# Kernel tuning notes

Measured on AMD Instinct MI355X. Metric: run time of the kernel, lower is better.

## Reference

```python
import jax, jax.numpy as jnp
import numpy as np

N = 50000      # number of genes
E = 1_600_000  # number of GRP edges
F = 256        # feature dim


def setup_inputs() -> dict:
    key = jax.random.key(0)
    k1, k2, k3 = jax.random.split(key, 3)
    indices = jax.random.randint(k1, (2, E), 0, N, dtype=jnp.int64 if jax.config.jax_enable_x64 else jnp.int32)
    values = jax.random.normal(k2, (E,), dtype=jnp.float32)
    mat_2 = jax.random.normal(k3, (N, F), dtype=jnp.float32)
    return {"indices": indices, "values": values, "n": N, "mat_2": mat_2}


def reference(indices, values, n, mat_2):
    # Sparse COO [n, n] @ dense [n, F]:
    # out[r] = sum over edges e with row[e]==r of values[e] * mat_2[col[e]]
    row, col = indices[0], indices[1]
    msgs = values[:, None] * mat_2[col]            # [E, F] gathered messages
    out = jax.ops.segment_sum(msgs, row, num_segments=n)  # [n, F]
    return out
```

## Files before the change

### kernel.cpp

```cpp
#include <hip/hip_runtime.h>

#define F_DIM   256
#define OVFCAP  8192
#define MAXBUCK 1024
#define BCAP    2560
#define P1_TILE 8192
#define NPASS   8
#define RCAP    24
#define ELLK    64

struct OvfEdge { int r, c; float v; };

__device__ __forceinline__ unsigned short f32_to_bf16(float x) {
    unsigned u = __float_as_uint(x);
    unsigned r = (u + 0x7FFFu + ((u >> 16) & 1u)) >> 16;
    return (unsigned short)r;
}

__device__ __forceinline__ void gfma(unsigned e, int lane,
                                     const unsigned short* __restrict__ mb, float4& acc) {
    int   col = (int)(e >> 16);
    float v   = __uint_as_float((e & 0xFFFFu) << 16);
    ushort4 m = ((const ushort4*)(mb + ((long long)col << 8)))[lane];
    acc.x += v * __uint_as_float((unsigned)m.x << 16);
    acc.y += v * __uint_as_float((unsigned)m.y << 16);
    acc.z += v * __uint_as_float((unsigned)m.z << 16);
    acc.w += v * __uint_as_float((unsigned)m.w << 16);
}

__global__ void cvt_kernel(const float* __restrict__ src,
                           unsigned short* __restrict__ dst, int n4) {
    int t = blockIdx.x * blockDim.x + threadIdx.x;
    if (t >= n4) return;
    float4 f = ((const float4*)src)[t];
    ushort4 o;
    o.x = f32_to_bf16(f.x); o.y = f32_to_bf16(f.y);
    o.z = f32_to_bf16(f.z); o.w = f32_to_bf16(f.w);
    ((ushort4*)dst)[t] = o;
}

__global__ void __launch_bounds__(1024)
build_kernel(const int* __restrict__ rows, const int* __restrict__ cols,
             const float* __restrict__ vals,
             const float* __restrict__ mat2, unsigned short* __restrict__ mb, int n4,
             int* __restrict__ gcur, int2* __restrict__ ebuf,
             int* __restrict__ ovfcnt, OvfEdge* __restrict__ ovf,
             int E, int nbuck, int p1blocks) {
    __shared__ int s_cnt[MAXBUCK];
    __shared__ int s_base[MAXBUCK];
    __shared__ int s_cur[MAXBUCK];
    const int t = threadIdx.x;
    const int bid = blockIdx.x;

    if (bid >= p1blocks) {
        int i = (bid - p1blocks) * 1024 + t;
        if (i < n4) {
            float4 f = ((const float4*)mat2)[i];
            ushort4 o;
            o.x = f32_to_bf16(f.x); o.y = f32_to_bf16(f.y);
            o.z = f32_to_bf16(f.z); o.w = f32_to_bf16(f.w);
            ((ushort4*)mb)[i] = o;
        }
        return;
    }

    for (int i = t; i < nbuck; i += 1024) { s_cnt[i] = 0; s_cur[i] = 0; }
    __syncthreads();

    const long long e0 = (long long)bid * P1_TILE;
    int4 r4[2], c4[2]; float4 v4[2];
    #pragma unroll
    for (int k = 0; k < 2; ++k) {
        long long i = e0 + (long long)k * 4096 + (long long)t * 4;
        if (i + 3 < E) {
            r4[k] = *(const int4*)(rows + i);
            c4[k] = *(const int4*)(cols + i);
            v4[k] = *(const float4*)(vals + i);
        } else {
            r4[k] = make_int4(-1, -1, -1, -1);
            c4[k] = make_int4(0, 0, 0, 0);
            v4[k] = make_float4(0.f, 0.f, 0.f, 0.f);
            #pragma unroll
            for (int j = 0; j < 4; ++j) {
                long long ii = i + j;
                if (ii < E) {
                    (&r4[k].x)[j] = rows[ii];
                    (&c4[k].x)[j] = cols[ii];
                    (&v4[k].x)[j] = vals[ii];
                }
            }
        }
        #pragma unroll
        for (int j = 0; j < 4; ++j) {
            int rr = (&r4[k].x)[j];
            if (rr >= 0) atomicAdd(&s_cnt[rr >> 6], 1);
        }
    }
    __syncthreads();
    for (int i = t; i < nbuck; i += 1024) {
        int c_ = s_cnt[i];
        s_base[i] = c_ ? atomicAdd(&gcur[i], c_) : 0;
    }
    __syncthreads();
    #pragma unroll
    for (int k = 0; k < 2; ++k) {
        #pragma unroll
        for (int j = 0; j < 4; ++j) {
            int rr = (&r4[k].x)[j];
            if (rr < 0) continue;
            int cc = (&c4[k].x)[j];
            float vv = (&v4[k].x)[j];
            int b = rr >> 6;
            int sl = s_base[b] + atomicAdd(&s_cur[b], 1);
            if (sl < BCAP) {
                ebuf[(long long)b * BCAP + sl] =
                    make_int2((int)(((unsigned)cc << 16) | f32_to_bf16(vv)), rr & 63);
            } else {
                int o = atomicAdd(ovfcnt, 1);
                if (o < OVFCAP) { ovf[o].r = rr; ovf[o].c = cc; ovf[o].v = vv; }
            }
        }
    }
}

__global__ void __launch_bounds__(512)
spmm_pass_kernel(const int* __restrict__ gcur, const int2* __restrict__ ebuf,
                 const unsigned short* __restrict__ mb,
                 float* __restrict__ out, int N,
                 int* __restrict__ ovfcnt, OvfEdge* __restrict__ ovf) {
    __shared__ int2 eds[BCAP];
    __shared__ unsigned ell_s[64 * RCAP];
    __shared__ int cur_s[64];
    const int t = threadIdx.x;
    const int b = blockIdx.x;
    const int cnt = min(gcur[b], BCAP);
    const int2* eb = ebuf + (long long)b * BCAP;
    for (int j = t; j < cnt; j += 512) eds[j] = eb[j];

    const int wid = t >> 6, lane = t & 63;
    float4 acc[8];
    #pragma unroll
    for (int r = 0; r < 8; ++r) acc[r] = make_float4(0.f, 0.f, 0.f, 0.f);

    const int passw = (N + NPASS - 1) / NPASS;

    for (int p = 0; p < NPASS; ++p) {
        if (t < 64) cur_s[t] = 0;
        __syncthreads();
        const int lo = p * passw;
        for (int j = t; j < cnt; j += 512) {
            int2 e = eds[j];
            int col = (int)((unsigned)e.x >> 16);
            if ((unsigned)(col - lo) < (unsigned)passw) {
                int pos = atomicAdd(&cur_s[e.y], 1);
                if (pos < RCAP) {
                    ell_s[e.y * RCAP + pos] = (unsigned)e.x;
                } else {
                    int o = atomicAdd(ovfcnt, 1);
                    if (o < OVFCAP) {
                        ovf[o].r = b * 64 + e.y;
                        ovf[o].c = col;
                        ovf[o].v = __uint_as_float(((unsigned)e.x & 0xFFFFu) << 16);
                    }
                }
            }
        }
        __syncthreads();
        #pragma unroll
        for (int ri = 0; ri < 8; ++ri) {
            const int rr = wid + (ri << 3);
            int deg = min(cur_s[rr], RCAP);
            unsigned pk = (lane < deg) ? ell_s[rr * RCAP + lane] : 0u;
            int padded = (deg + 3) & ~3;
            for (int j2 = 0; j2 < padded; j2 += 4) {
                #pragma unroll
                for (int k = 0; k < 4; ++k) {
                    unsigned e = (unsigned)__shfl((int)pk, j2 + k);
                    gfma(e, lane, mb, acc[ri]);
                }
            }
        }
        __syncthreads();
    }
    #pragma unroll
    for (int ri = 0; ri < 8; ++ri) {
        const int rr = wid + (ri << 3);
        long long gr = (long long)b * 64 + rr;
        if (gr < N) ((float4*)(out + (gr << 8)))[lane] = acc[ri];
    }
}

__global__ void ovf_kernel(const int* __restrict__ ovfcnt,
                           const OvfEdge* __restrict__ ovf,
                           const float* __restrict__ mat2,
                           float* __restrict__ out) {
    int cnt = min(*ovfcnt, OVFCAP);
    int lane = threadIdx.x & 63;
    int wid = threadIdx.x >> 6;
    for (int e = wid; e < cnt; e += 4) {
        OvfEdge ed = ovf[e];
        float4 m = ((const float4*)(mat2 + (long long)ed.c * F_DIM))[lane];
        float* dst = out + (long long)ed.r * F_DIM + lane * 4;
        unsafeAtomicAdd(dst + 0, ed.v * m.x);
        unsafeAtomicAdd(dst + 1, ed.v * m.y);
        unsafeAtomicAdd(dst + 2, ed.v * m.z);
        unsafeAtomicAdd(dst + 3, ed.v * m.w);
    }
}

__device__ __forceinline__ void scatter_one(int r, int c, float v,
                                            int* cursor, unsigned* ell,
                                            int* ovfcnt, OvfEdge* ovf) {
    int pos = atomicAdd(&cursor[r], 1);
    if (pos < ELLK) {
        ell[(long long)r * ELLK + pos] = ((unsigned)c << 16) | f32_to_bf16(v);
    } else {
        int o = atomicAdd(ovfcnt, 1);
        if (o < OVFCAP) { ovf[o].r = r; ovf[o].c = c; ovf[o].v = v; }
    }
}

__global__ void scatter_ell_kernel(const int* __restrict__ rows,
                                   const int* __restrict__ cols,
                                   const float* __restrict__ vals,
                                   int* __restrict__ cursor,
                                   unsigned* __restrict__ ell,
                                   int* __restrict__ ovfcnt,
                                   OvfEdge* __restrict__ ovf, int E) {
    int t = blockIdx.x * blockDim.x + threadIdx.x;
    int i0 = t * 4;
    if (i0 + 3 < E) {
        int4   r = *(const int4*)(rows + i0);
        int4   c = *(const int4*)(cols + i0);
        float4 v = *(const float4*)(vals + i0);
        scatter_one(r.x, c.x, v.x, cursor, ell, ovfcnt, ovf);
        scatter_one(r.y, c.y, v.y, cursor, ell, ovfcnt, ovf);
        scatter_one(r.z, c.z, v.z, cursor, ell, ovfcnt, ovf);
        scatter_one(r.w, c.w, v.w, cursor, ell, ovfcnt, ovf);
    } else {
        for (int i = i0; i < E; ++i)
            scatter_one(rows[i], cols[i], vals[i], cursor, ell, ovfcnt, ovf);
    }
}

template <bool BF16MAT>
__global__ void __launch_bounds__(256)
spmm_ell_kernel(const int* __restrict__ cursor,
                const unsigned* __restrict__ ell,
                const unsigned short* __restrict__ mb,
                const float* __restrict__ mat2,
                float* __restrict__ out, int N) {
    int wave = (int)(((long long)blockIdx.x * blockDim.x + threadIdx.x) >> 6);
    int lane = threadIdx.x & 63;
    if (wave >= N) return;
    int deg = min(cursor[wave], ELLK);
    unsigned pk = (lane < deg) ? ell[(long long)wave * ELLK + lane] : 0u;
    float4 acc = make_float4(0.f, 0.f, 0.f, 0.f);
    int padded = (deg + 7) & ~7;
    for (int j = 0; j < padded; j += 8) {
        #pragma unroll
        for (int k = 0; k < 8; ++k) {
            unsigned e = (unsigned)__shfl((int)pk, j + k);
            if (BF16MAT) {
                gfma(e, lane, mb, acc);
            } else {
                int   col = (int)(e >> 16);
                float v   = __uint_as_float((e & 0xFFFFu) << 16);
                float4 m = ((const float4*)(mat2 + ((long long)col << 8)))[lane];
                acc.x += v * m.x; acc.y += v * m.y;
                acc.z += v * m.z; acc.w += v * m.w;
            }
        }
    }
    ((float4*)(out + ((long long)wave << 8)))[lane] = acc;
}

__global__ void spmm_atomic_kernel(const int* __restrict__ rows,
                                   const int* __restrict__ cols,
                                   const float* __restrict__ vals,
                                   const float* __restrict__ mat2,
                                   float* __restrict__ out, int E) {
    long long gid = (long long)blockIdx.x * blockDim.x + threadIdx.x;
    long long e = gid >> 6;
    int q = (int)(gid & 63);
    if (e >= E) return;
    int r = rows[e]; int c = cols[e]; float v = vals[e];
    float4 m = ((const float4*)(mat2 + (long long)c * F_DIM))[q];
    float* dst = out + (long long)r * F_DIM + q * 4;
    unsafeAtomicAdd(dst + 0, v * m.x);
    unsafeAtomicAdd(dst + 1, v * m.y);
    unsafeAtomicAdd(dst + 2, v * m.z);
    unsafeAtomicAdd(dst + 3, v * m.w);
}

extern "C" void kernel_launch(void* const* d_in, const int* in_sizes, int n_in,
                              void* d_out, int out_size, void* d_ws, size_t ws_size,
                              hipStream_t stream) {
    const int*   indices = (const int*)d_in[0];
    const float* vals    = (const float*)d_in[1];
    const float* mat2    = (const float*)d_in[3];
    float*       out     = (float*)d_out;

    const int E  = in_sizes[1];
    const int N  = out_size / F_DIM;
    const int M2 = in_sizes[3];
    const int n4 = M2 / 4;
    const int* rows = indices;
    const int* cols = indices + E;
    const int nbuck = (N + 63) >> 6;

    auto align16 = [](size_t x) { return (x + 15) & ~(size_t)15; };
    char* ws = (char*)d_ws;

    size_t o = 0;
    int* gcur    = (int*)(ws + o);
    int* ovfcntA = gcur + nbuck;
    o = align16(o + ((size_t)nbuck + 1) * 4);
    OvfEdge* ovfA = (OvfEdge*)(ws + o); o = align16(o + (size_t)OVFCAP * sizeof(OvfEdge));
    int2* ebuf = (int2*)(ws + o);       o = align16(o + (size_t)nbuck * BCAP * 8);
    unsigned short* mbA = (unsigned short*)(ws + o); o = align16(o + (size_t)M2 * 2);
    size_t need_A = o;

    o = 0;
    int* cursor  = (int*)(ws + o);
    int* ovfcntB = cursor + N;
    o = align16(o + ((size_t)N + 1) * 4);
    OvfEdge* ovfB = (OvfEdge*)(ws + o); o = align16(o + (size_t)OVFCAP * sizeof(OvfEdge));
    unsigned* ellB = (unsigned*)(ws + o); o = align16(o + (size_t)N * ELLK * 4);
    size_t need_mid = o;
    unsigned short* mbB = (unsigned short*)(ws + o); o = align16(o + (size_t)M2 * 2);
    size_t need_full = o;

    const int vblocks = ((E + 3) / 4 + 255) / 256;
    const int sblocks = (N * 64 + 255) / 256;
    const int cblocks = (n4 + 255) / 256;
    const int p1blocks = (E + P1_TILE - 1) / P1_TILE;

    if (N <= 65535 && nbuck <= MAXBUCK && ws_size >= need_A) {
        hipMemsetAsync(gcur, 0, ((size_t)nbuck + 1) * 4, stream);
        int bgrid = p1blocks + (n4 + 1023) / 1024;
        build_kernel<<<bgrid, 1024, 0, stream>>>(rows, cols, vals, mat2, mbA, n4,
                                                 gcur, ebuf, ovfcntA, ovfA, E, nbuck, p1blocks);
        spmm_pass_kernel<<<nbuck, 512, 0, stream>>>(gcur, ebuf, mbA, out, N, ovfcntA, ovfA);
        ovf_kernel<<<1, 256, 0, stream>>>(ovfcntA, ovfA, mat2, out);
    } else if (N <= 65535 && ws_size >= need_full) {
        hipMemsetAsync(cursor, 0, ((size_t)N + 1) * 4, stream);
        cvt_kernel<<<cblocks, 256, 0, stream>>>(mat2, mbB, n4);
        scatter_ell_kernel<<<vblocks, 256, 0, stream>>>(rows, cols, vals, cursor, ellB, ovfcntB, ovfB, E);
        spmm_ell_kernel<true><<<sblocks, 256, 0, stream>>>(cursor, ellB, mbB, mat2, out, N);
        ovf_kernel<<<1, 256, 0, stream>>>(ovfcntB, ovfB, mat2, out);
    } else if (N <= 65535 && ws_size >= need_mid) {
        hipMemsetAsync(cursor, 0, ((size_t)N + 1) * 4, stream);
        scatter_ell_kernel<<<vblocks, 256, 0, stream>>>(rows, cols, vals, cursor, ellB, ovfcntB, ovfB, E);
        spmm_ell_kernel<false><<<sblocks, 256, 0, stream>>>(cursor, ellB, mbB, mat2, out, N);
        ovf_kernel<<<1, 256, 0, stream>>>(ovfcntB, ovfB, mat2, out);
    } else {
        hipMemsetAsync(d_out, 0, (size_t)out_size * sizeof(float), stream);
        long long total = (long long)E * 64;
        spmm_atomic_kernel<<<(int)((total + 255) / 256), 256, 0, stream>>>(rows, cols, vals, mat2, out, E);
    }
}
```

Before: 164.4 us.

## Double-buffer per-pass ELL binning and batch gather loads before FMAs

Restructures the multi-pass SpMM kernel so that binning edges for the next column pass into a second shared ELL buffer overlaps with the gather-FMA compute of the current pass. The inner loop now issues all four row gathers before accumulating, which exposes memory-level parallelism. Padding entries now point at a column inside the current pass window for cache locality. It also adds a launch-bounds occupancy hint and doubles the ELL shared memory, which may limit occupancy. A sync is still needed per pass for the buffer reset.

```diff
diff --git a/kernel.cpp b/kernel.cpp
--- a/kernel.cpp
+++ b/kernel.cpp
@@ -123,38 +123,33 @@
     }
 }
 
-__global__ void __launch_bounds__(512)
+__global__ void __launch_bounds__(512, 8)
 spmm_pass_kernel(const int* __restrict__ gcur, const int2* __restrict__ ebuf,
                  const unsigned short* __restrict__ mb,
                  float* __restrict__ out, int N,
                  int* __restrict__ ovfcnt, OvfEdge* __restrict__ ovf) {
     __shared__ int2 eds[BCAP];
-    __shared__ unsigned ell_s[64 * RCAP];
-    __shared__ int cur_s[64];
+    __shared__ unsigned ell_s[2][64 * RCAP];
+    __shared__ int cur_s[2][64];
     const int t = threadIdx.x;
     const int b = blockIdx.x;
     const int cnt = min(gcur[b], BCAP);
     const int2* eb = ebuf + (long long)b * BCAP;
     for (int j = t; j < cnt; j += 512) eds[j] = eb[j];
-
-    const int wid = t >> 6, lane = t & 63;
-    float4 acc[8];
-    #pragma unroll
-    for (int r = 0; r < 8; ++r) acc[r] = make_float4(0.f, 0.f, 0.f, 0.f);
+    if (t < 128) ((int*)cur_s)[t] = 0;
+    __syncthreads();
 
     const int passw = (N + NPASS - 1) / NPASS;
 
-    for (int p = 0; p < NPASS; ++p) {
-        if (t < 64) cur_s[t] = 0;
-        __syncthreads();
+    auto bin = [&](int p, int buf) {
         const int lo = p * passw;
         for (int j = t; j < cnt; j += 512) {
             int2 e = eds[j];
             int col = (int)((unsigned)e.x >> 16);
             if ((unsigned)(col - lo) < (unsigned)passw) {
-                int pos = atomicAdd(&cur_s[e.y], 1);
+                int pos = atomicAdd(&cur_s[buf][e.y], 1);
                 if (pos < RCAP) {
-                    ell_s[e.y * RCAP + pos] = (unsigned)e.x;
+                    ell_s[buf][e.y * RCAP + pos] = (unsigned)e.x;
                 } else {
                     int o = atomicAdd(ovfcnt, 1);
                     if (o < OVFCAP) {
@@ -165,23 +160,49 @@
                 }
             }
         }
-        __syncthreads();
+    };
+
+    bin(0, 0);
+    __syncthreads();
+
+    const int wid = t >> 6, lane = t & 63;
+    float4 acc[8];
+    #pragma unroll
+    for (int r = 0; r < 8; ++r) acc[r] = make_float4(0.f, 0.f, 0.f, 0.f);
+
+    for (int p = 0; p < NPASS; ++p) {
+        const int cur = p & 1, nxt = cur ^ 1;
+        if (p + 1 < NPASS) bin(p + 1, nxt);
+
+        const unsigned pad = (unsigned)(p * passw) << 16;
         #pragma unroll
         for (int ri = 0; ri < 8; ++ri) {
             const int rr = wid + (ri << 3);
-            int deg = min(cur_s[rr], RCAP);
-            unsigned pk = (lane < deg) ? ell_s[rr * RCAP + lane] : 0u;
+            int deg = min(cur_s[cur][rr], RCAP);
+            unsigned pk = (lane < deg) ? ell_s[cur][rr * RCAP + lane] : pad;
             int padded = (deg + 3) & ~3;
             for (int j2 = 0; j2 < padded; j2 += 4) {
+                ushort4 m[4]; float v[4];
                 #pragma unroll
                 for (int k = 0; k < 4; ++k) {
                     unsigned e = (unsigned)__shfl((int)pk, j2 + k);
-                    gfma(e, lane, mb, acc[ri]);
+                    v[k] = __uint_as_float((e & 0xFFFFu) << 16);
+                    m[k] = ((const ushort4*)(mb + ((long long)(e >> 16) << 8)))[lane];
                 }
+                #pragma unroll
+                for (int k = 0; k < 4; ++k) {
+                    acc[ri].x += v[k] * __uint_as_float((unsigned)m[k].x << 16);
+                    acc[ri].y += v[k] * __uint_as_float((unsigned)m[k].y << 16);
+                    acc[ri].z += v[k] * __uint_as_float((unsigned)m[k].z << 16);
+                    acc[ri].w += v[k] * __uint_as_float((unsigned)m[k].w << 16);
+                }
             }
         }
         __syncthreads();
-    }
+        if (t < 64) cur_s[cur][t] = 0;
+        __syncthreads();
+    }
+
     #pragma unroll
     for (int ri = 0; ri < 8; ++ri) {
         const int rr = wid + (ri << 3);
```

Measured after the change: 144.6 us (median of 2 runs). -12.1%, faster.

## Pre-sort bucket edges by column window and double-buffer ELL construction in SpMM pass

Applied to the files above, without the earlier changes.

Each block first counting-sorts its bucket's edges by column window in shared memory, so a pass only walks its own slice instead of rescanning all edges every pass. ELL tables are double-buffered so the next window's table is built while the current one is consumed, removing one barrier per pass. Rows are now handled by half-waves with 16-byte bf16 loads (8 features per lane), and a launch-bounds occupancy hint is added. The per-row ELL cap drops from 24 to 16 and windows become fixed 8192-column ranges, which may push more edges into the slower atomic overflow path.

```diff
diff --git a/kernel.cpp b/kernel.cpp
--- a/kernel.cpp
+++ b/kernel.cpp
@@ -5,8 +5,9 @@
 #define MAXBUCK 1024
 #define BCAP    2560
 #define P1_TILE 8192
-#define NPASS   8
-#define RCAP    24
+#define WINB    13
+#define MAXPASS 8
+#define RCAP2   16
 #define ELLK    64
 
 struct OvfEdge { int r, c; float v; };
@@ -123,70 +124,150 @@
     }
 }
 
-__global__ void __launch_bounds__(512)
+__global__ void __launch_bounds__(512, 6)
 spmm_pass_kernel(const int* __restrict__ gcur, const int2* __restrict__ ebuf,
                  const unsigned short* __restrict__ mb,
                  float* __restrict__ out, int N,
                  int* __restrict__ ovfcnt, OvfEdge* __restrict__ ovf) {
-    __shared__ int2 eds[BCAP];
-    __shared__ unsigned ell_s[64 * RCAP];
-    __shared__ int cur_s[64];
-    const int t = threadIdx.x;
-    const int b = blockIdx.x;
+    __shared__ int2 sorted[BCAP];
+    __shared__ unsigned ell_s[2][64 * RCAP2];
+    __shared__ int cur_s[2][64];
+    __shared__ int pcnt[8][MAXPASS];
+    __shared__ int pcur[8][MAXPASS];
+    __shared__ int soff[64];
+
+    const int t = threadIdx.x, b = blockIdx.x;
+    const int wid = t >> 6, lane = t & 63;
+    const int hw = t >> 5, fl = t & 31;
+    const int npass = (N + (1 << WINB) - 1) >> WINB;
     const int cnt = min(gcur[b], BCAP);
     const int2* eb = ebuf + (long long)b * BCAP;
-    for (int j = t; j < cnt; j += 512) eds[j] = eb[j];
-
-    const int wid = t >> 6, lane = t & 63;
-    float4 acc[8];
-    #pragma unroll
-    for (int r = 0; r < 8; ++r) acc[r] = make_float4(0.f, 0.f, 0.f, 0.f);
-
-    const int passw = (N + NPASS - 1) / NPASS;
-
-    for (int p = 0; p < NPASS; ++p) {
-        if (t < 64) cur_s[t] = 0;
-        __syncthreads();
-        const int lo = p * passw;
-        for (int j = t; j < cnt; j += 512) {
-            int2 e = eds[j];
-            int col = (int)((unsigned)e.x >> 16);
-            if ((unsigned)(col - lo) < (unsigned)passw) {
-                int pos = atomicAdd(&cur_s[e.y], 1);
-                if (pos < RCAP) {
-                    ell_s[e.y * RCAP + pos] = (unsigned)e.x;
-                } else {
+
+    if (t < 8 * MAXPASS) { ((int*)pcnt)[t] = 0; ((int*)pcur)[t] = 0; }
+    if (t < 128) ((int*)cur_s)[t] = 0;
+    #pragma unroll
+    for (int q = 0; q < (2 * 64 * RCAP2) / 512; ++q) ((unsigned*)ell_s)[t + q * 512] = 0u;
+    __syncthreads();
+
+    int2 e4[5]; int pid[5]; int nv = 0;
+    #pragma unroll
+    for (int k = 0; k < 5; ++k) {
+        int j = t + k * 512;
+        if (j < cnt) {
+            e4[nv] = eb[j];
+            pid[nv] = (int)((unsigned)e4[nv].x >> (16 + WINB));
+            atomicAdd(&pcnt[wid][pid[nv]], 1);
+            ++nv;
+        }
+    }
+    __syncthreads();
+
+    if (wid == 0) {
+        int val = pcnt[lane & 7][lane >> 3];
+        int x = val;
+        #pragma unroll
+        for (int off = 1; off < 64; off <<= 1) {
+            int y = __shfl_up(x, off);
+            if (lane >= off) x += y;
+        }
+        soff[lane] = x - val;
+    }
+    __syncthreads();
+
+    for (int k = 0; k < nv; ++k) {
+        int p = pid[k];
+        int pos = atomicAdd(&pcur[wid][p], 1);
+        sorted[soff[p * 8 + wid] + pos] = e4[k];
+    }
+    __syncthreads();
+
+    {
+        int beg = soff[0];
+        int end = (npass > 1) ? soff[8] : cnt;
+        for (int j = beg + t; j < end; j += 512) {
+            int2 e = sorted[j];
+            int pos = atomicAdd(&cur_s[0][e.y], 1);
+            if (pos < RCAP2) ell_s[0][(e.y << 4) | pos] = (unsigned)e.x;
+            else {
+                int o = atomicAdd(ovfcnt, 1);
+                if (o < OVFCAP) {
+                    ovf[o].r = b * 64 + e.y;
+                    ovf[o].c = (int)((unsigned)e.x >> 16);
+                    ovf[o].v = __uint_as_float(((unsigned)e.x & 0xFFFFu) << 16);
+                }
+            }
+        }
+    }
+    __syncthreads();
+
+    float acc[4][8];
+    #pragma unroll
+    for (int r = 0; r < 4; ++r)
+        #pragma unroll
+        for (int q = 0; q < 8; ++q) acc[r][q] = 0.f;
+
+    for (int p = 0; p < npass; ++p) {
+        const int cur = p & 1, nxt = cur ^ 1;
+
+        if (p + 1 < npass) {
+            int beg = soff[(p + 1) * 8];
+            int end = (p + 2 < npass) ? soff[(p + 2) * 8] : cnt;
+            for (int j = beg + t; j < end; j += 512) {
+                int2 e = sorted[j];
+                int pos = atomicAdd(&cur_s[nxt][e.y], 1);
+                if (pos < RCAP2) ell_s[nxt][(e.y << 4) | pos] = (unsigned)e.x;
+                else {
                     int o = atomicAdd(ovfcnt, 1);
                     if (o < OVFCAP) {
                         ovf[o].r = b * 64 + e.y;
-                        ovf[o].c = col;
+                        ovf[o].c = (int)((unsigned)e.x >> 16);
                         ovf[o].v = __uint_as_float(((unsigned)e.x & 0xFFFFu) << 16);
                     }
                 }
             }
         }
-        __syncthreads();
-        #pragma unroll
-        for (int ri = 0; ri < 8; ++ri) {
-            const int rr = wid + (ri << 3);
-            int deg = min(cur_s[rr], RCAP);
-            unsigned pk = (lane < deg) ? ell_s[rr * RCAP + lane] : 0u;
+
+        #pragma unroll
+        for (int ri = 0; ri < 4; ++ri) {
+            const int rr = hw + (ri << 4);
+            int deg = min(cur_s[cur][rr], RCAP2);
             int padded = (deg + 3) & ~3;
-            for (int j2 = 0; j2 < padded; j2 += 4) {
+            for (int j = 0; j < padded; j += 4) {
+                int4 m[4]; float v[4];
                 #pragma unroll
                 for (int k = 0; k < 4; ++k) {
-                    unsigned e = (unsigned)__shfl((int)pk, j2 + k);
-                    gfma(e, lane, mb, acc[ri]);
+                    unsigned e = ell_s[cur][(rr << 4) + j + k];
+                    v[k] = __uint_as_float((e & 0xFFFFu) << 16);
+                    m[k] = ((const int4*)(mb + ((long long)(e >> 16) << 8)))[fl];
                 }
-            }
+                #pragma unroll
+                for (int k = 0; k < 4; ++k) {
+                    acc[ri][0] += v[k] * __uint_as_float((unsigned)m[k].x << 16);
+                    acc[ri][1] += v[k] * __uint_as_float((unsigned)m[k].x & 0xFFFF0000u);
+                    acc[ri][2] += v[k] * __uint_as_float((unsigned)m[k].y << 16);
+                    acc[ri][3] += v[k] * __uint_as_float((unsigned)m[k].y & 0xFFFF0000u);
+                    acc[ri][4] += v[k] * __uint_as_float((unsigned)m[k].z << 16);
+                    acc[ri][5] += v[k] * __uint_as_float((unsigned)m[k].z & 0xFFFF0000u);
+                    acc[ri][6] += v[k] * __uint_as_float((unsigned)m[k].w << 16);
+                    acc[ri][7] += v[k] * __uint_as_float((unsigned)m[k].w & 0xFFFF0000u);
+                }
+            }
+            #pragma unroll
+            for (int z = fl; z < RCAP2; z += 32) ell_s[cur][(rr << 4) + z] = 0u;
+            if (fl == 0) cur_s[cur][rr] = 0;
         }
         __syncthreads();
     }
-    #pragma unroll
-    for (int ri = 0; ri < 8; ++ri) {
-        const int rr = wid + (ri << 3);
+
+    #pragma unroll
+    for (int ri = 0; ri < 4; ++ri) {
+        const int rr = hw + (ri << 4);
         long long gr = (long long)b * 64 + rr;
-        if (gr < N) ((float4*)(out + (gr << 8)))[lane] = acc[ri];
+        if (gr < N) {
+            float4* op = (float4*)(out + (gr << 8) + (fl << 3));
+            op[0] = make_float4(acc[ri][0], acc[ri][1], acc[ri][2], acc[ri][3]);
+            op[1] = make_float4(acc[ri][4], acc[ri][5], acc[ri][6], acc[ri][7]);
+        }
     }
 }
 
```

Result: slower. 175.9 us (+7.0%).
